# Kernel optimization log

Hardware: AMD Instinct MI355X
Metric: run time of the kernel (lower is better)

The kernel has to match this reference:

```python
import jax, jax.numpy as jnp
import numpy as np

TEMP = 0.05
ALPHA = 0.1
EPS = 1e-12


def setup_inputs() -> dict:
    key = jax.random.key(0)
    k1, k2, k3, k4 = jax.random.split(key, 4)
    bs, emb_dim, n_class, n_aux = 16384, 512, 2000, 5
    features = jax.random.normal(k1, (bs, emb_dim), dtype=jnp.float32)
    word_embed = jax.random.normal(k2, (n_class, emb_dim), dtype=jnp.float32)
    label = jax.random.randint(k3, (bs,), 0, n_class)
    aux = jax.random.randint(k4, (bs, n_aux), 0, n_class)
    return {"features": features, "word_embed": word_embed, "label": label, "aux": aux}


def _cosine_logits(features, word_embed):
    # F.normalize(x, dim=-1): x / max(||x||, eps)
    f = features / jnp.maximum(jnp.linalg.norm(features, axis=-1, keepdims=True), EPS)
    w = word_embed / jnp.maximum(jnp.linalg.norm(word_embed, axis=-1, keepdims=True), EPS)
    return jnp.matmul(f, w.T) / TEMP  # (bs, n_class)


def reference(features, word_embed, label, aux):
    pred = _cosine_logits(features, word_embed)
    lse = jax.nn.logsumexp(pred, axis=1)                                  # log sum exp per row
    tgt = jnp.take_along_axis(pred, label[:, None], axis=1)[:, 0]         # pred[i, target[i]]
    # normal cross entropy: mean_i(-pred[i,t_i] + log sum exp(pred[i]))
    loss_normal = jnp.mean(-tgt + lse)
    # label-smoothing CE: -(1-a)*pred[i,t_i] + lse - (a/n_aux)*sum_j pred[i, aux[i,j]]
    single_alpha = ALPHA / aux.shape[-1]
    aux_logits = jnp.take_along_axis(pred, aux, axis=1)                   # (bs, n_aux)
    loss_ls = jnp.mean(-(1.0 - ALPHA) * tgt + lse - single_alpha * jnp.sum(aux_logits, axis=1))
    loss = 0.5 * (loss_normal + loss_ls)
    acc = jnp.mean((jnp.argmax(pred, axis=1) == label).astype(jnp.float32))
    return loss, acc
```

## Files before the change

kernel.cpp:

```cpp
#include <hip/hip_runtime.h>
#include <hip/hip_bf16.h>
#include <hip/hip_fp8.h>
#include <stdint.h>

#define BS   16384
#define NC   2000
#define NCP  2048
#define EMB  512
#define NAUX 5
#define NCHUNK 32
#define GBLK 4096

typedef __bf16 bf16x8 __attribute__((ext_vector_type(8)));
typedef float  f32x4  __attribute__((ext_vector_type(4)));

__global__ __launch_bounds__(256) void norm_kernel(
    const float* __restrict__ feat, const float* __restrict__ wemb,
    unsigned char* __restrict__ fn8, unsigned char* __restrict__ wn8,
    __bf16* __restrict__ fnb, __bf16* __restrict__ wnb)
{
    const int lane = threadIdx.x & 63;
    const int wv   = threadIdx.x >> 6;
    const int row  = blockIdx.x * 4 + wv;

    if (row >= BS + NC) {
        const int pr = row - BS;
        *(unsigned*)(wn8 + (size_t)pr * EMB + lane * 4)       = 0u;
        *(unsigned*)(wn8 + (size_t)pr * EMB + 256 + lane * 4) = 0u;
        ushort4 z = {0, 0, 0, 0};
        ((ushort4*)(wnb + (size_t)pr * EMB))[lane]      = z;
        ((ushort4*)(wnb + (size_t)pr * EMB))[64 + lane] = z;
        return;
    }
    const float* src;
    unsigned char* dst8;
    __bf16* dstb;
    if (row < BS) { src = feat + (size_t)row * EMB;
                    dst8 = fn8 + (size_t)row * EMB;        dstb = fnb + (size_t)row * EMB; }
    else          { src = wemb + (size_t)(row - BS) * EMB;
                    dst8 = wn8 + (size_t)(row - BS) * EMB; dstb = wnb + (size_t)(row - BS) * EMB; }

    const float4* s4 = (const float4*)src;
    float4 x = s4[lane];
    float4 y = s4[64 + lane];

    float ss = x.x * x.x + x.y * x.y + x.z * x.z + x.w * x.w
             + y.x * y.x + y.y * y.y + y.z * y.z + y.w * y.w;
    #pragma unroll
    for (int m = 1; m < 64; m <<= 1) ss += __shfl_xor(ss, m, 64);
    const float scale = 1.0f / fmaxf(sqrtf(ss), 1e-12f);

    float v[8];
    v[0] = x.x * scale; v[1] = x.y * scale; v[2] = x.z * scale; v[3] = x.w * scale;
    v[4] = y.x * scale; v[5] = y.y * scale; v[6] = y.z * scale; v[7] = y.w * scale;

    __bf16 b[8];
    #pragma unroll
    for (int j = 0; j < 8; ++j) b[j] = (__bf16)v[j];
    *(ushort4*)(dstb + 4 * lane)       = *(const ushort4*)(b);
    *(ushort4*)(dstb + 256 + 4 * lane) = *(const ushort4*)(b + 4);

    int p0 = 0, p1 = 0;
    p0 = __builtin_amdgcn_cvt_pk_fp8_f32(v[0], v[1], p0, false);
    p0 = __builtin_amdgcn_cvt_pk_fp8_f32(v[2], v[3], p0, true);
    p1 = __builtin_amdgcn_cvt_pk_fp8_f32(v[4], v[5], p1, false);
    p1 = __builtin_amdgcn_cvt_pk_fp8_f32(v[6], v[7], p1, true);
    *(int*)(dst8 + 4 * lane)       = p0;
    *(int*)(dst8 + 256 + 4 * lane) = p1;
}

__global__ __launch_bounds__(256) void main_kernel(
    const unsigned char* __restrict__ fn8, const unsigned char* __restrict__ wn8,
    float* __restrict__ es_p, unsigned* __restrict__ key_p)
{
    __shared__ __align__(16) unsigned char As[2][8192];
    __shared__ __align__(16) unsigned char Bs[2][8192];

    const int tid   = threadIdx.x;
    const int lane  = tid & 63;
    const int l15   = lane & 15;
    const int quad  = lane >> 4;
    const int wv    = tid >> 6;
    const int wvM   = wv >> 1;
    const int wvN   = wv & 1;
    const int xcd   = blockIdx.x & 7;
    const int j     = blockIdx.x >> 3;
    const int mTile = xcd * 16 + (j >> 4);
    const int nTile = j & 15;

    const unsigned char* fbase = fn8 + (size_t)mTile * 128 * EMB;
    const unsigned char* wbase = wn8 + (size_t)nTile * 128 * EMB;

    const int r8   = lane >> 3;
    const int chv  = (lane & 7) ^ r8;
    const int gc16 = chv & 3;
    const int rowB = r8 * 2 + (chv >> 2);

    f32x4 acc[4][4] = {};

    auto STAGE = [&](int t, int buf) {
        #pragma unroll
        for (int p = 0; p < 2; ++p) {
            const int slot = wv * 2 + p;
            const int grow = slot * 16 + rowB;
            const size_t goff = (size_t)grow * EMB + (size_t)t * 64 + (size_t)gc16 * 16;
            __builtin_amdgcn_global_load_lds(
                (const __attribute__((address_space(1))) void*)(fbase + goff),
                (__attribute__((address_space(3))) void*)(&As[buf][slot * 1024]), 16, 0, 0);
            __builtin_amdgcn_global_load_lds(
                (const __attribute__((address_space(1))) void*)(wbase + goff),
                (__attribute__((address_space(3))) void*)(&Bs[buf][slot * 1024]), 16, 0, 0);
        }
    };

    STAGE(0, 0);
    STAGE(1, 1);

    #pragma unroll
    for (int t = 0; t < 8; ++t) {
        if (t < 7) asm volatile("s_waitcnt vmcnt(4)" ::: "memory");
        else       asm volatile("s_waitcnt vmcnt(0)" ::: "memory");
        __builtin_amdgcn_s_barrier();

        const int cur = t & 1;
        #pragma unroll
        for (int kc = 0; kc < 2; ++kc) {
            long aF[4], bF[4];
            const int c16  = kc * 2 + (quad >> 1);
            const int hoff = (quad & 1) << 3;
            #pragma unroll
            for (int i = 0; i < 4; ++i) {
                const int ar = wvM * 64 + i * 16 + l15;
                const int br = wvN * 64 + i * 16 + l15;
                const int pa = ((((ar & 1) << 2) + c16) ^ ((ar >> 1) & 7)) * 16 + hoff;
                const int pb = ((((br & 1) << 2) + c16) ^ ((br >> 1) & 7)) * 16 + hoff;
                aF[i] = *(const long*)(&As[cur][(ar >> 1) * 128 + pa]);
                bF[i] = *(const long*)(&Bs[cur][(br >> 1) * 128 + pb]);
            }
            #pragma unroll
            for (int mi = 0; mi < 4; ++mi)
                #pragma unroll
                for (int ni = 0; ni < 4; ++ni)
                    acc[mi][ni] = __builtin_amdgcn_mfma_f32_16x16x32_fp8_fp8(
                        aF[mi], bF[ni], acc[mi][ni], 0, 0, 0);
        }

        if (t < 6) {
            asm volatile("s_waitcnt lgkmcnt(0)" ::: "memory");
            __builtin_amdgcn_s_barrier();
            STAGE(t + 2, cur);
        }
    }

    const float C20 = 28.853900817779268f;
    const int chunk = nTile * 2 + wvN;
    #pragma unroll
    for (int mi = 0; mi < 4; ++mi) {
        float    es[4] = {0.f, 0.f, 0.f, 0.f};
        unsigned km[4] = {0u, 0u, 0u, 0u};
        #pragma unroll
        for (int ni = 0; ni < 4; ++ni) {
            const int col = nTile * 128 + wvN * 64 + ni * 16 + l15;
            const unsigned colenc = 2047u - (unsigned)col;
            const bool valid = (col < NC);
            #pragma unroll
            for (int r = 0; r < 4; ++r) {
                float v = valid ? acc[mi][ni][r] : -3.0f;
                es[r] += exp2f((v - 1.0f) * C20);
                unsigned u = __float_as_uint(v);
                unsigned k = u ^ (unsigned)(((int)u >> 31) | 0x80000000);
                unsigned pk = (k & 0xFFFFF800u) | colenc;
                km[r] = pk > km[r] ? pk : km[r];
            }
        }
        #pragma unroll
        for (int r = 0; r < 4; ++r) {
            #pragma unroll
            for (int m = 1; m < 16; m <<= 1) {
                es[r] += __shfl_xor(es[r], m, 64);
                unsigned x = __shfl_xor(km[r], m, 64);
                km[r] = x > km[r] ? x : km[r];
            }
        }
        if (l15 == 0) {
            #pragma unroll
            for (int r = 0; r < 4; ++r) {
                const int row = mTile * 128 + wvM * 64 + mi * 16 + quad * 4 + r;
                es_p [(size_t)row * NCHUNK + chunk] = es[r];
                key_p[(size_t)row * NCHUNK + chunk] = km[r];
            }
        }
    }
}

__global__ __launch_bounds__(256) void gather_fin_kernel(
    const __bf16* __restrict__ fnb, const __bf16* __restrict__ wnb,
    const int* __restrict__ label, const int* __restrict__ aux,
    const float* __restrict__ es_p, const unsigned* __restrict__ key_p,
    float* __restrict__ blkpart)
{
    const int lane = threadIdx.x & 63;
    const int wv   = threadIdx.x >> 6;
    const int row  = blockIdx.x * 4 + wv;

    const int cch = lane & 31;
    float    es = es_p [(size_t)row * NCHUNK + cch];
    unsigned k  = key_p[(size_t)row * NCHUNK + cch];

    const int lab = label[row];
    int cols[6];
    cols[0] = lab;
    #pragma unroll
    for (int j = 0; j < NAUX; ++j) cols[j + 1] = aux[row * NAUX + j];

    bf16x8 f8 = *((const bf16x8*)fnb + (size_t)row * (EMB / 8) + lane);

    bf16x8 w8[6];
    #pragma unroll
    for (int c = 0; c < 6; ++c)
        w8[c] = *((const bf16x8*)wnb + (size_t)cols[c] * (EMB / 8) + lane);

    float fv[8];
    #pragma unroll
    for (int j = 0; j < 8; ++j) fv[j] = (float)f8[j];

    float d[6];
    #pragma unroll
    for (int c = 0; c < 6; ++c) {
        float t = 0.f;
        #pragma unroll
        for (int j = 0; j < 8; ++j) t += fv[j] * (float)w8[c][j];
        d[c] = t;
    }

    #pragma unroll
    for (int m = 1; m < 64; m <<= 1) {
        #pragma unroll
        for (int c = 0; c < 6; ++c) d[c] += __shfl_xor(d[c], m, 64);
        if (m < 32) {
            es += __shfl_xor(es, m, 64);
            unsigned x = __shfl_xor(k, m, 64);
            k = x > k ? x : k;
        }
    }

    const float tgt  = d[0] * 20.0f;
    const float auxs = (d[1] + d[2] + d[3] + d[4] + d[5]) * 20.0f;
    const int amax = 2047 - (int)(k & 0x7FFu);
    const float loss = 20.0f + logf(es) - 0.95f * tgt - 0.01f * auxs;
    const float acc  = (amax == lab) ? 1.0f : 0.0f;

    __shared__ float sl[4], sa[4];
    if (lane == 0) { sl[wv] = loss; sa[wv] = acc; }
    __syncthreads();
    if (threadIdx.x == 0) {
        blkpart[blockIdx.x]        = sl[0] + sl[1] + sl[2] + sl[3];
        blkpart[GBLK + blockIdx.x] = sa[0] + sa[1] + sa[2] + sa[3];
    }
}

__global__ __launch_bounds__(256) void fin2_kernel(
    const float* __restrict__ blkpart, float* __restrict__ out)
{
    float l = 0.f, a = 0.f;
    #pragma unroll
    for (int i = 0; i < GBLK / 256; ++i) {
        l += blkpart[i * 256 + threadIdx.x];
        a += blkpart[GBLK + i * 256 + threadIdx.x];
    }
    #pragma unroll
    for (int m = 1; m < 64; m <<= 1) {
        l += __shfl_xor(l, m, 64);
        a += __shfl_xor(a, m, 64);
    }
    __shared__ float sl[4], sa[4];
    const int wv = threadIdx.x >> 6;
    if ((threadIdx.x & 63) == 0) { sl[wv] = l; sa[wv] = a; }
    __syncthreads();
    if (threadIdx.x == 0) {
        out[0] = (sl[0] + sl[1] + sl[2] + sl[3]) / (float)BS;
        out[1] = (sa[0] + sa[1] + sa[2] + sa[3]) / (float)BS;
    }
}

extern "C" void kernel_launch(void* const* d_in, const int* in_sizes, int n_in,
                              void* d_out, int out_size, void* d_ws, size_t ws_size,
                              hipStream_t stream)
{
    const float* feat  = (const float*)d_in[0];
    const float* wemb  = (const float*)d_in[1];
    const int*   label = (const int*)d_in[2];
    const int*   aux   = (const int*)d_in[3];

    char* ws = (char*)d_ws;
    unsigned char* fn8     = (unsigned char*)(ws);
    unsigned char* wn8     = (unsigned char*)(ws + 8388608);
    __bf16*        fnb     = (__bf16*)(ws + 9437184);
    __bf16*        wnb     = (__bf16*)(ws + 26214400);
    float*         es_p    = (float*)(ws + 28311552);
    unsigned*      key_p   = (unsigned*)(ws + 30408704);
    float*         blkpart = (float*)(ws + 32505856);
    float*         out     = (float*)d_out;

    hipLaunchKernelGGL(norm_kernel, dim3((BS + NCP) / 4), dim3(256), 0, stream,
                       feat, wemb, fn8, wn8, fnb, wnb);
    hipLaunchKernelGGL(main_kernel, dim3((BS / 128) * (NCP / 128)), dim3(256), 0, stream,
                       fn8, wn8, es_p, key_p);
    hipLaunchKernelGGL(gather_fin_kernel, dim3(GBLK), dim3(256), 0, stream,
                       fnb, wnb, label, aux, es_p, key_p, blkpart);
    hipLaunchKernelGGL(fin2_kernel, dim3(1), dim3(256), 0, stream, blkpart, out);
}
```

Before: 133.5 us.

## Enlarge GEMM tile to 256x256 with 8 waves and triple-buffered LDS

The main fp8 MFMA kernel moves from 128x128 tiles with 4 waves to 256x256 tiles with 8 waves, which doubles per-block operand reuse and halves grid size. It switches from double to triple buffering and interleaves the global-to-LDS staging with the MFMA phases, using barriers, sched_barrier and setprio to overlap loads and compute. LDS use grows to 96KB per block and accumulators double per wave. The grid drops to 512 blocks, which may underfill the GPU's CUs, and the extra barriers add sync overhead.

```diff
diff --git a/kernel.cpp b/kernel.cpp
--- a/kernel.cpp
+++ b/kernel.cpp
@@ -69,98 +69,109 @@
     *(int*)(dst8 + 256 + 4 * lane) = p1;
 }
 
-__global__ __launch_bounds__(256) void main_kernel(
+__global__ __launch_bounds__(512, 2) void main_kernel(
     const unsigned char* __restrict__ fn8, const unsigned char* __restrict__ wn8,
     float* __restrict__ es_p, unsigned* __restrict__ key_p)
 {
-    __shared__ __align__(16) unsigned char As[2][8192];
-    __shared__ __align__(16) unsigned char Bs[2][8192];
+    __shared__ __align__(16) unsigned char As[3][16384];
+    __shared__ __align__(16) unsigned char Bs[3][16384];
 
     const int tid   = threadIdx.x;
     const int lane  = tid & 63;
     const int l15   = lane & 15;
     const int quad  = lane >> 4;
     const int wv    = tid >> 6;
-    const int wvM   = wv >> 1;
-    const int wvN   = wv & 1;
+    const int wvM   = wv >> 2;
+    const int wvN   = wv & 3;
     const int xcd   = blockIdx.x & 7;
     const int j     = blockIdx.x >> 3;
-    const int mTile = xcd * 16 + (j >> 4);
-    const int nTile = j & 15;
-
-    const unsigned char* fbase = fn8 + (size_t)mTile * 128 * EMB;
-    const unsigned char* wbase = wn8 + (size_t)nTile * 128 * EMB;
+    const int mTile = xcd * 8 + (j >> 3);
+    const int nTile = j & 7;
+
+    const unsigned char* fbase = fn8 + (size_t)mTile * 256 * EMB;
+    const unsigned char* wbase = wn8 + (size_t)nTile * 256 * EMB;
 
     const int r8   = lane >> 3;
     const int chv  = (lane & 7) ^ r8;
     const int gc16 = chv & 3;
     const int rowB = r8 * 2 + (chv >> 2);
-
-    f32x4 acc[4][4] = {};
-
-    auto STAGE = [&](int t, int buf) {
-        #pragma unroll
-        for (int p = 0; p < 2; ++p) {
-            const int slot = wv * 2 + p;
-            const int grow = slot * 16 + rowB;
-            const size_t goff = (size_t)grow * EMB + (size_t)t * 64 + (size_t)gc16 * 16;
-            __builtin_amdgcn_global_load_lds(
-                (const __attribute__((address_space(1))) void*)(fbase + goff),
-                (__attribute__((address_space(3))) void*)(&As[buf][slot * 1024]), 16, 0, 0);
-            __builtin_amdgcn_global_load_lds(
-                (const __attribute__((address_space(1))) void*)(wbase + goff),
-                (__attribute__((address_space(3))) void*)(&Bs[buf][slot * 1024]), 16, 0, 0);
-        }
+    const int hoff = (quad & 1) << 3;
+
+    f32x4 acc[8][4] = {};
+
+    auto STAGE_A = [&](int t, int buf, int p) {
+        const int slot = wv * 2 + p;
+        const int grow = slot * 16 + rowB;
+        const size_t goff = (size_t)grow * EMB + (size_t)t * 64 + (size_t)gc16 * 16;
+        __builtin_amdgcn_global_load_lds(
+            (const __attribute__((address_space(1))) void*)(fbase + goff),
+            (__attribute__((address_space(3))) void*)(&As[buf][slot * 1024]), 16, 0, 0);
     };
-
-    STAGE(0, 0);
-    STAGE(1, 1);
+    auto STAGE_B = [&](int t, int buf, int p) {
+        const int slot = wv * 2 + p;
+        const int grow = slot * 16 + rowB;
+        const size_t goff = (size_t)grow * EMB + (size_t)t * 64 + (size_t)gc16 * 16;
+        __builtin_amdgcn_global_load_lds(
+            (const __attribute__((address_space(1))) void*)(wbase + goff),
+            (__attribute__((address_space(3))) void*)(&Bs[buf][slot * 1024]), 16, 0, 0);
+    };
+
+    STAGE_A(0, 0, 0); STAGE_A(0, 0, 1); STAGE_B(0, 0, 0); STAGE_B(0, 0, 1);
+    STAGE_A(1, 1, 0); STAGE_A(1, 1, 1); STAGE_B(1, 1, 0); STAGE_B(1, 1, 1);
+    asm volatile("s_waitcnt vmcnt(4)" ::: "memory");
+    __builtin_amdgcn_s_barrier();
 
     #pragma unroll
     for (int t = 0; t < 8; ++t) {
-        if (t < 7) asm volatile("s_waitcnt vmcnt(4)" ::: "memory");
-        else       asm volatile("s_waitcnt vmcnt(0)" ::: "memory");
-        __builtin_amdgcn_s_barrier();
-
-        const int cur = t & 1;
-        #pragma unroll
-        for (int kc = 0; kc < 2; ++kc) {
+        const int cur  = t % 3;
+        const int nxt2 = (t + 2) % 3;
+        #pragma unroll
+        for (int p = 0; p < 4; ++p) {
+            const int kc  = p >> 1;
+            const int mh  = p & 1;
+            const int c16 = kc * 2 + (quad >> 1);
             long aF[4], bF[4];
-            const int c16  = kc * 2 + (quad >> 1);
-            const int hoff = (quad & 1) << 3;
             #pragma unroll
             for (int i = 0; i < 4; ++i) {
-                const int ar = wvM * 64 + i * 16 + l15;
+                const int ar = wvM * 128 + (mh * 4 + i) * 16 + l15;
                 const int br = wvN * 64 + i * 16 + l15;
                 const int pa = ((((ar & 1) << 2) + c16) ^ ((ar >> 1) & 7)) * 16 + hoff;
                 const int pb = ((((br & 1) << 2) + c16) ^ ((br >> 1) & 7)) * 16 + hoff;
                 aF[i] = *(const long*)(&As[cur][(ar >> 1) * 128 + pa]);
                 bF[i] = *(const long*)(&Bs[cur][(br >> 1) * 128 + pb]);
             }
-            #pragma unroll
-            for (int mi = 0; mi < 4; ++mi)
+            if (t < 6) {
+                if (p < 2) STAGE_A(t + 2, nxt2, p);
+                else       STAGE_B(t + 2, nxt2, p - 2);
+            }
+            if (p == 3) {
+                if (t < 6)       asm volatile("s_waitcnt vmcnt(4)" ::: "memory");
+                else if (t == 6) asm volatile("s_waitcnt vmcnt(0)" ::: "memory");
+            }
+            __builtin_amdgcn_s_barrier();
+            asm volatile("s_waitcnt lgkmcnt(0)" ::: "memory");
+            __builtin_amdgcn_sched_barrier(0);
+            __builtin_amdgcn_s_setprio(1);
+            #pragma unroll
+            for (int i = 0; i < 4; ++i)
                 #pragma unroll
                 for (int ni = 0; ni < 4; ++ni)
-                    acc[mi][ni] = __builtin_amdgcn_mfma_f32_16x16x32_fp8_fp8(
-                        aF[mi], bF[ni], acc[mi][ni], 0, 0, 0);
-        }
-
-        if (t < 6) {
-            asm volatile("s_waitcnt lgkmcnt(0)" ::: "memory");
+                    acc[mh * 4 + i][ni] = __builtin_amdgcn_mfma_f32_16x16x32_fp8_fp8(
+                        aF[i], bF[ni], acc[mh * 4 + i][ni], 0, 0, 0);
+            __builtin_amdgcn_s_setprio(0);
             __builtin_amdgcn_s_barrier();
-            STAGE(t + 2, cur);
         }
     }
 
     const float C20 = 28.853900817779268f;
-    const int chunk = nTile * 2 + wvN;
-    #pragma unroll
-    for (int mi = 0; mi < 4; ++mi) {
+    const int chunk = nTile * 4 + wvN;
+    #pragma unroll
+    for (int mi = 0; mi < 8; ++mi) {
         float    es[4] = {0.f, 0.f, 0.f, 0.f};
         unsigned km[4] = {0u, 0u, 0u, 0u};
         #pragma unroll
         for (int ni = 0; ni < 4; ++ni) {
-            const int col = nTile * 128 + wvN * 64 + ni * 16 + l15;
+            const int col = nTile * 256 + wvN * 64 + ni * 16 + l15;
             const unsigned colenc = 2047u - (unsigned)col;
             const bool valid = (col < NC);
             #pragma unroll
@@ -185,7 +196,7 @@
         if (l15 == 0) {
             #pragma unroll
             for (int r = 0; r < 4; ++r) {
-                const int row = mTile * 128 + wvM * 64 + mi * 16 + quad * 4 + r;
+                const int row = mTile * 256 + wvM * 128 + mi * 16 + quad * 4 + r;
                 es_p [(size_t)row * NCHUNK + chunk] = es[r];
                 key_p[(size_t)row * NCHUNK + chunk] = km[r];
             }
@@ -304,7 +315,7 @@
 
     hipLaunchKernelGGL(norm_kernel, dim3((BS + NCP) / 4), dim3(256), 0, stream,
                        feat, wemb, fn8, wn8, fnb, wnb);
-    hipLaunchKernelGGL(main_kernel, dim3((BS / 128) * (NCP / 128)), dim3(256), 0, stream,
+    hipLaunchKernelGGL(main_kernel, dim3((BS / 256) * (NCP / 256)), dim3(512), 0, stream,
                        fn8, wn8, es_p, key_p);
     hipLaunchKernelGGL(gather_fin_kernel, dim3(GBLK), dim3(256), 0, stream,
                        fnb, wnb, label, aux, es_p, key_p, blkpart);
```

Result: slower. 145.8 us (+9.2%).
